# Performance work log

Hardware: AMD Instinct MI355X
Metric: run time of the kernel (lower is better)

Reference implementation:

```python
import jax, jax.numpy as jnp
import numpy as np

DT = 0.01          # oscillator integration step
GPI_TAU = 0.01     # gpi accumulation rate
NOISE_TAU = 1.0    # noise scale
MIN_OMEGA, MAX_OMEGA = 0.1, 1.0


def clinear(xr, xi, Wr, Wi, br, bi):
    # complex linear: (Wr + i Wi)(xr + i xi) + (br + i bi), weights stored [out, in]
    yr = xr @ Wr.T - xi @ Wi.T + br
    yi = xr @ Wi.T + xi @ Wr.T + bi
    return yr, yi


def crelu(yr, yi):
    # ReLU applied to real and imaginary parts independently
    return jax.nn.relu(yr), jax.nn.relu(yi)


def hopf_step(xr, xi, r, phi, omega):
    # Hopf oscillator in polar form, forced by complex input x = xr + i xi:
    #   dr   = dt * ( r(1 - r^2) + Re(x e^{-i phi}) )
    #   dphi = dt * ( omega + Im(x e^{-i phi}) / r )
    # output = r_new * e^{i phi_new}
    c, s = jnp.cos(phi), jnp.sin(phi)
    r_new = r + DT * (r * (1.0 - r * r) + xr * c + xi * s)
    phi_new = phi + DT * (omega + (xi * c - xr * s) / jnp.maximum(r, 1e-6))
    return r_new * jnp.cos(phi_new), r_new * jnp.sin(phi_new), r_new, phi_new


def setup_inputs() -> dict:
    T, D, U, A = 4096, 256, 2048, 64
    key = jax.random.key(0)
    ks = jax.random.split(key, 16)

    def lin(k, out_d, in_d):
        k1, k2, k3, k4 = jax.random.split(k, 4)
        sc = 1.0 / np.sqrt(in_d)
        return (jax.random.normal(k1, (out_d, in_d), dtype=jnp.float32) * sc,
                jax.random.normal(k2, (out_d, in_d), dtype=jnp.float32) * sc,
                jax.random.normal(k3, (out_d,), dtype=jnp.float32) * sc,
                jax.random.normal(k4, (out_d,), dtype=jnp.float32) * sc)

    l1Wr, l1Wi, l1br, l1bi = lin(ks[0], U, D)
    dpWr, dpWi, dpbr, dpbi = lin(ks[1], A, U)
    ipWr, ipWi, ipbr, ipbi = lin(ks[2], A, U)
    cWr, cWi, cbr, cbi = lin(ks[3], 1, U)
    return {
        'state': jax.random.normal(ks[4], (T, 1, D), dtype=jnp.float32),
        'phi1_init': jax.random.uniform(ks[5], (1, U), dtype=jnp.float32),
        'phi2_init': jax.random.uniform(ks[6], (1, U), dtype=jnp.float32),
        'noise_u': jax.random.uniform(ks[7], (T, A), dtype=jnp.float32),
        'omega1': jax.random.uniform(ks[8], (U,), minval=MIN_OMEGA, maxval=MAX_OMEGA, dtype=jnp.float32),
        'omega2': jax.random.uniform(ks[9], (U,), minval=MIN_OMEGA, maxval=MAX_OMEGA, dtype=jnp.float32),
        'l1Wr': l1Wr, 'l1Wi': l1Wi, 'l1br': l1br, 'l1bi': l1bi,
        'dpWr': dpWr, 'dpWi': dpWi, 'dpbr': dpbr, 'dpbi': dpbi,
        'ipWr': ipWr, 'ipWi': ipWi, 'ipbr': ipbr, 'ipbi': ipbi,
        'cWr': cWr, 'cWi': cWi, 'cbr': cbr, 'cbi': cbi,
    }


def reference(state, phi1_init, phi2_init, noise_u, omega1, omega2,
              l1Wr, l1Wi, l1br, l1bi, dpWr, dpWi, dpbr, dpbi,
              ipWr, ipWi, ipbr, ipbi, cWr, cWi, cbr, cbi):
    U = l1Wr.shape[0]
    A = dpWr.shape[0]
    carry0 = (jnp.ones((1, U)), phi1_init * 0.1,   # r1, phi1 (torch.rand/10)
              jnp.ones((1, U)), phi2_init * 0.1,   # r2, phi2
              jnp.zeros((1, A)),                   # gpi
              jnp.zeros((1, 1)))                   # p_value

    def step(carry, xs):
        r1, phi1, r2, phi2, gpi, p_value = carry
        s_t, nz_t = xs  # s_t: [1, D], nz_t: [A]
        # x = cReLU(l1(complex(state[t], state[t])))
        xr, xi = crelu(*clinear(s_t, s_t, l1Wr, l1Wi, l1br, l1bi))
        d1r, d1i, r1, phi1 = hopf_step(xr, xi, r1, phi1, omega1)
        d2r, d2i, r2, phi2 = hopf_step(xr, xi, r2, phi2, omega2)
        vr, vi = clinear(d1r, d1i, cWr, cWi, cbr, cbi)
        value = jnp.sqrt(vr * vr + vi * vi)          # |critic(d1out)|  [1,1]
        delta_V = value - p_value                    # pd_flag = sc_flag = 0
        lD1 = jax.nn.sigmoid(5.0 * delta_V)
        lD2 = jax.nn.sigmoid(-5.0 * delta_V)
        dpr, dpi = crelu(*clinear(d1r * lD1, d1i * lD1, dpWr, dpWi, dpbr, dpbi))
        ipr, ipi = crelu(*clinear(d2r * lD2, d2i * lD2, ipWr, ipWi, ipbr, ipbi))
        noise = NOISE_TAU * (nz_t[None, :] * 2.0 * lD2 - lD2)  # real-valued, adds to real part
        diff_r = dpr - (ipr + noise)
        diff_i = dpi - ipi
        gpi = gpi + GPI_TAU * jnp.sqrt(diff_r * diff_r + diff_i * diff_i)
        return (r1, phi1, r2, phi2, gpi, value), (gpi, value)

    (r1, phi1, r2, phi2, gpi, value), (gpi_traj, value_traj) = jax.lax.scan(
        step, carry0, (state, noise_u))
    probs = jax.nn.softmax(gpi, axis=1)
    return probs, value, gpi_traj
```

## Files before the change

### kernel.cpp

```cpp
#include <hip/hip_runtime.h>
#include <hip/hip_bf16.h>
#include <string.h>
#include <stdint.h>


#define T_ 4096
#define D_ 256
#define U_ 2048
#define A_ 64

typedef float f32x4 __attribute__((ext_vector_type(4)));
typedef short bh8 __attribute__((ext_vector_type(8)));
union F8 { uint32_t u[4]; bh8 v; };

__device__ __forceinline__ float bflo(uint32_t p) { return __uint_as_float(p << 16); }
__device__ __forceinline__ float bfhi(uint32_t p) { return __uint_as_float(p & 0xffff0000u); }
__device__ __forceinline__ uint16_t bf16rne(float x) {
  __hip_bfloat16 h = __float2bfloat16(x);
  uint16_t u;
  __builtin_memcpy(&u, &h, 2);
  return u;
}

#define HOPF_LOAD(BUF, i, tbase)                                            \
  do {                                                                      \
    const float* bx_ = xc + (size_t)((tbase) + (i)) * (U_ * 2);             \
    asm volatile("global_load_dwordx2 %0, %1, %2"                           \
                 : "=v"(BUF[i])                                             \
                 : "v"(voffx), "s"(bx_));                                   \
  } while (0)

#define HOPF_STEP(BUF, i, tb)                                               \
  do {                                                                      \
    const float xr_ = BUF[i].x, xi_ = BUF[i].y;                             \
    const float f_ = fmaf(xr_, c, xi_ * s);                                 \
    const float g_ = fmaf(xi_, c, -(xr_ * s));                              \
    const float rn_ = fmaf(0.01f, fmaf(r, fmaf(-r, r, 1.0f), f_), r);       \
    const float rinv_ = __builtin_amdgcn_rcpf(fmaxf(r, 1e-6f));             \
    const float phin_ = fmaf(0.01f, g_ * rinv_, phi + dto);                 \
    float cn_, sn_;                                                         \
    __sincosf(phin_, &sn_, &cn_);                                           \
    uint32_t pk_;                                                           \
    asm("v_cvt_pk_bf16_f32 %0, %1, %2"                                     \
        : "=v"(pk_)                                                         \
        : "v"(rn_ * cn_), "v"(rn_ * sn_));                                  \
    const uint32_t* bd_ = dst + (size_t)((tb) + (i)) * U_;                  \
    asm volatile("global_store_dword %0, %1, %2" ::"v"(voffd), "v"(pk_),    \
                 "s"(bd_));                                                  \
    r = rn_; phi = phin_; c = cn_; s = sn_;                                 \
  } while (0)

#define VMWAIT(N)                                  \
  asm volatile("s_waitcnt vmcnt(" #N ")");         \
  __builtin_amdgcn_sched_barrier(0)

#define WAIT_TILE(tt)                                                       \
  do {                                                                      \
    uint32_t rdy_;                                                          \
    for (;;) {                                                              \
      rdy_ = 0u;                                                            \
      if (threadIdx.x == 0)                                                 \
        rdy_ = __hip_atomic_fetch_add(&flags[tt], 0u, __ATOMIC_RELAXED,     \
                                      __HIP_MEMORY_SCOPE_AGENT);            \
      rdy_ = __shfl(rdy_, 0);                                               \
      if (rdy_ >= 32u) break;                                               \
      __builtin_amdgcn_s_sleep(8);                                          \
    }                                                                       \
    __builtin_amdgcn_sched_barrier(0);                                      \
  } while (0)

__global__ __launch_bounds__(256) void k_fused(
    const float* __restrict__ S, const float* __restrict__ Wr,
    const float* __restrict__ Wi, const float* __restrict__ br,
    const float* __restrict__ bi, const float* __restrict__ phi1,
    const float* __restrict__ phi2, const float* __restrict__ om1,
    const float* __restrict__ om2, float* __restrict__ xc,
    uint32_t* __restrict__ d1c, uint32_t* __restrict__ d2c,
    uint32_t* __restrict__ flags) {
  const int bid = blockIdx.x;
  if (bid >= 64) {
    __shared__ float sT[32][68];
    __shared__ float wrT[32][68];
    __shared__ float wiT[32][68];
    const int tid = threadIdx.x;
    const int gb = bid - 64;
    const int t0 = (gb >> 5) * 64;
    const int u0 = (gb & 31) * 64;
    const int un = tid & 15, tm = tid >> 4;
    const int lr = tid >> 3;
    const int lc = (tid & 7) * 4;
    float accR[4][4] = {}, accI[4][4] = {};
    for (int k0 = 0; k0 < D_; k0 += 32) {
      __syncthreads();
#pragma unroll
      for (int p = 0; p < 2; ++p) {
        const int row = p * 32 + lr;
        float4 v = *(const float4*)&S[(size_t)(t0 + row) * D_ + k0 + lc];
        sT[lc + 0][row] = v.x; sT[lc + 1][row] = v.y;
        sT[lc + 2][row] = v.z; sT[lc + 3][row] = v.w;
        float4 a = *(const float4*)&Wr[(size_t)(u0 + row) * D_ + k0 + lc];
        wrT[lc + 0][row] = a.x; wrT[lc + 1][row] = a.y;
        wrT[lc + 2][row] = a.z; wrT[lc + 3][row] = a.w;
        float4 b = *(const float4*)&Wi[(size_t)(u0 + row) * D_ + k0 + lc];
        wiT[lc + 0][row] = b.x; wiT[lc + 1][row] = b.y;
        wiT[lc + 2][row] = b.z; wiT[lc + 3][row] = b.w;
      }
      __syncthreads();
#pragma unroll
      for (int k = 0; k < 32; ++k) {
        const float4 sv = *(const float4*)&sT[k][tm * 4];
        const float4 ar = *(const float4*)&wrT[k][un * 4];
        const float4 ai = *(const float4*)&wiT[k][un * 4];
        const float ss[4] = {sv.x, sv.y, sv.z, sv.w};
        const float wd[4] = {ar.x - ai.x, ar.y - ai.y, ar.z - ai.z, ar.w - ai.w};
        const float wm[4] = {ar.x + ai.x, ar.y + ai.y, ar.z + ai.z, ar.w + ai.w};
#pragma unroll
        for (int i = 0; i < 4; ++i)
#pragma unroll
          for (int j = 0; j < 4; ++j) {
            accR[i][j] = fmaf(ss[i], wd[j], accR[i][j]);
            accI[i][j] = fmaf(ss[i], wm[j], accI[i][j]);
          }
      }
    }
    const float4 brv = *(const float4*)&br[u0 + un * 4];
    const float4 biv = *(const float4*)&bi[u0 + un * 4];
    const float brx[4] = {brv.x, brv.y, brv.z, brv.w};
    const float bix[4] = {biv.x, biv.y, biv.z, biv.w};
#pragma unroll
    for (int i = 0; i < 4; ++i) {
      float vr[4], vi[4];
#pragma unroll
      for (int j = 0; j < 4; ++j) {
        vr[j] = fmaxf(accR[i][j] + brx[j], 0.f);
        vi[j] = fmaxf(accI[i][j] + bix[j], 0.f);
      }
      const size_t base = ((size_t)(t0 + tm * 4 + i) * U_ + u0 + un * 4) * 2;
      f32x4 lo = {vr[0], vi[0], vr[1], vi[1]};
      f32x4 hi = {vr[2], vi[2], vr[3], vi[3]};
      float* p0 = &xc[base];
      float* p1 = &xc[base + 4];
      asm volatile("global_store_dwordx4 %0, %1, off sc1" ::"v"(p0), "v"(lo)
                   : "memory");
      asm volatile("global_store_dwordx4 %0, %1, off sc1" ::"v"(p1), "v"(hi)
                   : "memory");
    }
    asm volatile("s_waitcnt vmcnt(0)");
    __syncthreads();
    if (tid == 0)
      __hip_atomic_fetch_add(&flags[t0 >> 6], 1u, __ATOMIC_RELAXED,
                             __HIP_MEMORY_SCOPE_AGENT);
    return;
  }
  if (threadIdx.x >= 64) return;
  __builtin_amdgcn_s_setprio(3);
  const int ub = bid & 31;
  const int osc = bid >> 5;
  const int u = ub * 64 + threadIdx.x;
  float phi = (osc ? phi2[u] : phi1[u]) * 0.1f;
  const float omega = osc ? om2[u] : om1[u];
  const uint32_t* __restrict__ dst = (osc ? d2c : d1c);
  const float dto = 0.01f * omega;
  float r = 1.0f;
  float c, s;
  __sincosf(phi, &s, &c);
  const uint32_t voffx = (uint32_t)u * 8u;
  const uint32_t voffd = (uint32_t)u * 4u;

  constexpr int PF = 32;
  float2 bufA[PF], bufB[PF];
  WAIT_TILE(0);
#pragma unroll
  for (int i = 0; i < PF; ++i) HOPF_LOAD(bufA, i, 0);
#pragma unroll
  for (int i = 0; i < PF; ++i) HOPF_LOAD(bufB, i, PF);
  VMWAIT(32);

  for (int t0 = 0; t0 < T_; t0 += 2 * PF) {
#pragma unroll
    for (int i = 0; i < PF; ++i) HOPF_STEP(bufA, i, t0);
    {
      int tp = t0 + 2 * PF;
      if (tp >= T_) tp = 0;
      WAIT_TILE(tp >> 6);
#pragma unroll
      for (int i = 0; i < PF; ++i) HOPF_LOAD(bufA, i, tp);
    }
    VMWAIT(63);
#pragma unroll
    for (int i = 0; i < PF; ++i) HOPF_STEP(bufB, i, t0 + PF);
    {
      int tp = t0 + 3 * PF;
      if (tp >= T_) tp = 0;
#pragma unroll
      for (int i = 0; i < PF; ++i) HOPF_LOAD(bufB, i, tp);
    }
    VMWAIT(63);
  }
  asm volatile("s_waitcnt vmcnt(0)");
  __builtin_amdgcn_s_setprio(0);
}

__global__ __launch_bounds__(256) void k_crit_wcvt(
    const uint32_t* __restrict__ d1c, const float* __restrict__ cWr,
    const float* __restrict__ cWi, const float* __restrict__ cbr,
    const float* __restrict__ cbi, const float* __restrict__ dpWr,
    const float* __restrict__ dpWi, const float* __restrict__ ipWr,
    const float* __restrict__ ipWi, float* __restrict__ value,
    uint16_t* __restrict__ wc) {
  const int tid = threadIdx.x;
  if (blockIdx.x >= T_) {
    const float* srcs[4] = {dpWr, dpWi, ipWr, ipWi};
    const int g = (blockIdx.x - T_) * 256 + tid;
#pragma unroll
    for (int mi = 0; mi < 4; ++mi) {
      const float* sp = srcs[mi];
      uint16_t* hi = wc + (size_t)(2 * mi) * 131072;
      uint16_t* lo = wc + (size_t)(2 * mi + 1) * 131072;
      for (int j = 0; j < 32; ++j) {
        const int e = g * 32 + j;
        const float w = sp[e];
        const uint16_t hb = bf16rne(w);
        const float hf = __uint_as_float((uint32_t)hb << 16);
        hi[e] = hb;
        lo[e] = bf16rne(w - hf);
      }
    }
    return;
  }
  const int t = blockIdx.x;
  float vr = 0.f, vi = 0.f;
#pragma unroll
  for (int i = 0; i < 8; ++i) {
    const int uu = i * 256 + tid;
    const uint32_t p = d1c[(size_t)t * U_ + uu];
    const float dr = bflo(p), di = bfhi(p);
    const float wr = cWr[uu], wi = cWi[uu];
    vr = fmaf(dr, wr, fmaf(-di, wi, vr));
    vi = fmaf(dr, wi, fmaf(di, wr, vi));
  }
#pragma unroll
  for (int o = 32; o >= 1; o >>= 1) {
    vr += __shfl_xor(vr, o);
    vi += __shfl_xor(vi, o);
  }
  __shared__ float red[2][4];
  if ((tid & 63) == 0) { red[0][tid >> 6] = vr; red[1][tid >> 6] = vi; }
  __syncthreads();
  if (tid == 0) {
    const float r0 = red[0][0] + red[0][1] + red[0][2] + red[0][3] + cbr[0];
    const float i0 = red[1][0] + red[1][1] + red[1][2] + red[1][3] + cbi[0];
    value[t] = sqrtf(r0 * r0 + i0 * i0);
  }
}

#define MFMA_(A, B, C) \
  __builtin_amdgcn_mfma_f32_16x16x32_bf16((A).v, (B).v, (C), 0, 0, 0)

__global__ __launch_bounds__(256) void k_gemmDm_ld(
    const uint32_t* __restrict__ d1c, const uint32_t* __restrict__ d2c,
    const uint16_t* __restrict__ wc, const float* __restrict__ value,
    float* __restrict__ m, float* __restrict__ lD1,
    float* __restrict__ lD2) {
  const int tid = threadIdx.x;
  const int bid = blockIdx.x;
  if (bid >= 256) {
    const int t = (bid - 256) * 256 + tid;
    const float v = value[t];
    const float pv = (t > 0) ? value[t - 1] : 0.f;
    const float x = 5.0f * (v - pv);
    const float sg = 1.0f / (1.0f + __expf(-x));
    lD1[t] = sg;
    lD2[t] = 1.0f - sg;
    return;
  }
  const int w = tid >> 6;
  const int l = tid & 63;
  const int t0 = bid * 16;
  const int a0 = w * 16;
  const int lr15 = l & 15;
  const int g4 = (l >> 4) * 4;
  const uint32_t* d1p = d1c + (size_t)(t0 + lr15) * U_ + g4;
  const uint32_t* d2p = d2c + (size_t)(t0 + lr15) * U_ + g4;
  const size_t wbase = (size_t)(a0 + lr15) * U_ + g4;
  const uint16_t* w0 = wc + wbase;
  f32x4 acc0 = {0.f, 0.f, 0.f, 0.f};
  f32x4 acc1 = {0.f, 0.f, 0.f, 0.f};
  f32x4 acc2 = {0.f, 0.f, 0.f, 0.f};
  f32x4 acc3 = {0.f, 0.f, 0.f, 0.f};
  for (int kk = 0; kk < U_; kk += 32) {
    const uint4 da = *(const uint4*)(d1p + kk);
    const uint4 db = *(const uint4*)(d1p + kk + 16);
    F8 fr1, fi1, f1n;
    fr1.u[0] = (da.x & 0xffffu) | (da.y << 16);
    fr1.u[1] = (da.z & 0xffffu) | (da.w << 16);
    fr1.u[2] = (db.x & 0xffffu) | (db.y << 16);
    fr1.u[3] = (db.z & 0xffffu) | (db.w << 16);
    fi1.u[0] = (da.x >> 16) | (da.y & 0xffff0000u);
    fi1.u[1] = (da.z >> 16) | (da.w & 0xffff0000u);
    fi1.u[2] = (db.x >> 16) | (db.y & 0xffff0000u);
    fi1.u[3] = (db.z >> 16) | (db.w & 0xffff0000u);
    f1n.u[0] = fi1.u[0] ^ 0x80008000u; f1n.u[1] = fi1.u[1] ^ 0x80008000u;
    f1n.u[2] = fi1.u[2] ^ 0x80008000u; f1n.u[3] = fi1.u[3] ^ 0x80008000u;
    const uint4 dc = *(const uint4*)(d2p + kk);
    const uint4 dd = *(const uint4*)(d2p + kk + 16);
    F8 fr2, fi2, f2n;
    fr2.u[0] = (dc.x & 0xffffu) | (dc.y << 16);
    fr2.u[1] = (dc.z & 0xffffu) | (dc.w << 16);
    fr2.u[2] = (dd.x & 0xffffu) | (dd.y << 16);
    fr2.u[3] = (dd.z & 0xffffu) | (dd.w << 16);
    fi2.u[0] = (dc.x >> 16) | (dc.y & 0xffff0000u);
    fi2.u[1] = (dc.z >> 16) | (dc.w & 0xffff0000u);
    fi2.u[2] = (dd.x >> 16) | (dd.y & 0xffff0000u);
    fi2.u[3] = (dd.z >> 16) | (dd.w & 0xffff0000u);
    f2n.u[0] = fi2.u[0] ^ 0x80008000u; f2n.u[1] = fi2.u[1] ^ 0x80008000u;
    f2n.u[2] = fi2.u[2] ^ 0x80008000u; f2n.u[3] = fi2.u[3] ^ 0x80008000u;
    F8 wf[8];
#pragma unroll
    for (int ai = 0; ai < 8; ++ai) {
      const uint16_t* bp = w0 + (size_t)ai * 131072 + kk;
      const uint2 x0 = *(const uint2*)bp;
      const uint2 x1 = *(const uint2*)(bp + 16);
      wf[ai].u[0] = x0.x; wf[ai].u[1] = x0.y;
      wf[ai].u[2] = x1.x; wf[ai].u[3] = x1.y;
    }
    acc0 = MFMA_(fr1, wf[0], acc0); acc0 = MFMA_(fr1, wf[1], acc0);
    acc0 = MFMA_(f1n, wf[2], acc0); acc0 = MFMA_(f1n, wf[3], acc0);
    acc1 = MFMA_(fr1, wf[2], acc1); acc1 = MFMA_(fr1, wf[3], acc1);
    acc1 = MFMA_(fi1, wf[0], acc1); acc1 = MFMA_(fi1, wf[1], acc1);
    acc2 = MFMA_(fr2, wf[4], acc2); acc2 = MFMA_(fr2, wf[5], acc2);
    acc2 = MFMA_(f2n, wf[6], acc2); acc2 = MFMA_(f2n, wf[7], acc2);
    acc3 = MFMA_(fr2, wf[6], acc3); acc3 = MFMA_(fr2, wf[7], acc3);
    acc3 = MFMA_(fi2, wf[4], acc3); acc3 = MFMA_(fi2, wf[5], acc3);
  }
  const size_t MS = (size_t)T_ * A_;
#pragma unroll
  for (int reg = 0; reg < 4; ++reg) {
    const int t = t0 + (l >> 4) * 4 + reg;
    const size_t o = (size_t)t * A_ + a0 + lr15;
    m[0 * MS + o] = acc0[reg];
    m[1 * MS + o] = acc1[reg];
    m[2 * MS + o] = acc2[reg];
    m[3 * MS + o] = acc3[reg];
  }
}

__global__ __launch_bounds__(256) void k_epi(
    const float* __restrict__ m4, const float* __restrict__ lD1,
    const float* __restrict__ lD2, const float* __restrict__ noise,
    const float* __restrict__ dpbr, const float* __restrict__ dpbi,
    const float* __restrict__ ipbr, const float* __restrict__ ipbi,
    float* __restrict__ nrm) {
  const size_t MS = (size_t)T_ * A_;
  const int gid = blockIdx.x * 256 + threadIdx.x;
  const size_t e0 = (size_t)gid * 4;
  const int t = (int)(e0 >> 6);
  const int a0 = (int)(e0 & 63);
  float m[4][4];
#pragma unroll
  for (int mi = 0; mi < 4; ++mi) {
    const float4 v = *(const float4*)&m4[(size_t)mi * MS + e0];
    m[mi][0] = v.x; m[mi][1] = v.y; m[mi][2] = v.z; m[mi][3] = v.w;
  }
  const float l1 = lD1[t], l2 = lD2[t];
  const float4 nzv = *(const float4*)&noise[e0];
  const float nz[4] = {nzv.x, nzv.y, nzv.z, nzv.w};
  const float4 q1 = *(const float4*)&dpbr[a0];
  const float4 q2 = *(const float4*)&dpbi[a0];
  const float4 q3 = *(const float4*)&ipbr[a0];
  const float4 q4 = *(const float4*)&ipbi[a0];
  const float b1r[4] = {q1.x, q1.y, q1.z, q1.w};
  const float b1i[4] = {q2.x, q2.y, q2.z, q2.w};
  const float b2r[4] = {q3.x, q3.y, q3.z, q3.w};
  const float b2i[4] = {q4.x, q4.y, q4.z, q4.w};
  float res[4];
#pragma unroll
  for (int j = 0; j < 4; ++j) {
    const float dpr = fmaxf(fmaf(l1, m[0][j], b1r[j]), 0.f);
    const float dpi = fmaxf(fmaf(l1, m[1][j], b1i[j]), 0.f);
    const float ipr = fmaxf(fmaf(l2, m[2][j], b2r[j]), 0.f);
    const float ipi = fmaxf(fmaf(l2, m[3][j], b2i[j]), 0.f);
    const float nzs = l2 * (2.f * nz[j] - 1.f);
    const float dr = dpr - ipr - nzs;
    const float di = dpi - ipi;
    res[j] = sqrtf(dr * dr + di * di);
  }
  *(float4*)&nrm[e0] = make_float4(res[0], res[1], res[2], res[3]);
}

__global__ __launch_bounds__(64) void k_scan_part(const float* __restrict__ nrm,
                                                  float* __restrict__ csum) {
  const int c = blockIdx.x;
  const int a = threadIdx.x;
  const int tb = c * 64;
  float run = 0.f;
  for (int i = 0; i < 64; ++i) run += nrm[(size_t)(tb + i) * 64 + a];
  csum[c * 64 + a] = run;
}

__global__ __launch_bounds__(64) void k_scan_mid(const float* __restrict__ csum,
                                                 const float* __restrict__ value,
                                                 float* __restrict__ coff,
                                                 float* __restrict__ out) {
  const int a = threadIdx.x;
  float acc = 0.f;
#pragma unroll
  for (int cc = 0; cc < 64; ++cc) {
    coff[cc * 64 + a] = acc;
    acc += csum[cc * 64 + a];
  }
  const float g = 0.01f * acc;
  float mx = g;
#pragma unroll
  for (int o = 32; o >= 1; o >>= 1) mx = fmaxf(mx, __shfl_xor(mx, o));
  const float e = __expf(g - mx);
  float sm = e;
#pragma unroll
  for (int o = 32; o >= 1; o >>= 1) sm += __shfl_xor(sm, o);
  out[a] = e / sm;
  if (a == 0) out[64] = value[T_ - 1];
}

__global__ __launch_bounds__(64) void k_scan_out(const float* __restrict__ nrm,
                                                 const float* __restrict__ coff,
                                                 float* __restrict__ out) {
  const int c = blockIdx.x;
  const int a = threadIdx.x;
  const int tb = c * 64;
  float off = coff[c * 64 + a];
  float* o65 = out + 65;
  for (int i = 0; i < 64; ++i) {
    off += nrm[(size_t)(tb + i) * 64 + a];
    o65[(size_t)(tb + i) * 64 + a] = 0.01f * off;
  }
}

extern "C" void kernel_launch(void* const* d_in, const int* in_sizes, int n_in,
                              void* d_out, int out_size, void* d_ws,
                              size_t ws_size, hipStream_t stream) {
  const float* state = (const float*)d_in[0];
  const float* phi1 = (const float*)d_in[1];
  const float* phi2 = (const float*)d_in[2];
  const float* noise = (const float*)d_in[3];
  const float* om1 = (const float*)d_in[4];
  const float* om2 = (const float*)d_in[5];
  const float* l1Wr = (const float*)d_in[6];
  const float* l1Wi = (const float*)d_in[7];
  const float* l1br = (const float*)d_in[8];
  const float* l1bi = (const float*)d_in[9];
  const float* dpWr = (const float*)d_in[10];
  const float* dpWi = (const float*)d_in[11];
  const float* dpbr = (const float*)d_in[12];
  const float* dpbi = (const float*)d_in[13];
  const float* ipWr = (const float*)d_in[14];
  const float* ipWi = (const float*)d_in[15];
  const float* ipbr = (const float*)d_in[16];
  const float* ipbi = (const float*)d_in[17];
  const float* cWr = (const float*)d_in[18];
  const float* cWi = (const float*)d_in[19];
  const float* cbr = (const float*)d_in[20];
  const float* cbi = (const float*)d_in[21];
  float* out = (float*)d_out;

  char* ws = (char*)d_ws;
  float* xc = (float*)(ws + (size_t)0);
  uint32_t* d1c = (uint32_t*)(ws + (size_t)67108864);
  uint32_t* d2c = (uint32_t*)(ws + (size_t)100663296);
  float* m4 = (float*)(ws + (size_t)0);
  uint16_t* wc = (uint16_t*)(ws + (size_t)4194304);
  float* nrm = (float*)(ws + (size_t)16777216);
  float* value = (float*)(ws + (size_t)17825792);
  float* lD1 = (float*)(ws + (size_t)17825792 + 16384);
  float* lD2 = (float*)(ws + (size_t)17825792 + 32768);
  float* csum = (float*)(ws + (size_t)17825792 + 49152);
  float* coff = (float*)(ws + (size_t)17825792 + 65536);
  uint32_t* flags = (uint32_t*)out;

  hipMemsetAsync(out, 0, 256, stream);
  k_fused<<<64 + (T_ / 64) * (U_ / 64), 256, 0, stream>>>(
      state, l1Wr, l1Wi, l1br, l1bi, phi1, phi2, om1, om2, xc, d1c, d2c,
      flags);
  k_crit_wcvt<<<T_ + 16, 256, 0, stream>>>(d1c, cWr, cWi, cbr, cbi, dpWr,
                                           dpWi, ipWr, ipWi, value, wc);
  k_gemmDm_ld<<<256 + 16, 256, 0, stream>>>(d1c, d2c, wc, value, m4, lD1,
                                            lD2);
  k_epi<<<256, 256, 0, stream>>>(m4, lD1, lD2, noise, dpbr, dpbi, ipbr, ipbi,
                                 nrm);
  k_scan_part<<<64, 64, 0, stream>>>(nrm, csum);
  k_scan_mid<<<1, 64, 0, stream>>>(csum, value, coff, out);
  k_scan_out<<<64, 64, 0, stream>>>(nrm, coff, out);
}
```

Measured before the change: 543.3 us.

## Pre-swizzle split-bf16 weights into fragment order and stage activations via LDS

```diff
diff --git a/kernel.cpp b/kernel.cpp
--- a/kernel.cpp
+++ b/kernel.cpp
@@ -211,20 +211,43 @@
   const int tid = threadIdx.x;
   if (blockIdx.x >= T_) {
     const float* srcs[4] = {dpWr, dpWi, ipWr, ipWi};
-    const int g = (blockIdx.x - T_) * 256 + tid;
-#pragma unroll
-    for (int mi = 0; mi < 4; ++mi) {
-      const float* sp = srcs[mi];
-      uint16_t* hi = wc + (size_t)(2 * mi) * 131072;
-      uint16_t* lo = wc + (size_t)(2 * mi + 1) * 131072;
-      for (int j = 0; j < 32; ++j) {
-        const int e = g * 32 + j;
-        const float w = sp[e];
-        const uint16_t hb = bf16rne(w);
-        const float hf = __uint_as_float((uint32_t)hb << 16);
-        hi[e] = hb;
-        lo[e] = bf16rne(w - hf);
-      }
+    const int wgid = (blockIdx.x - T_) * 4 + (tid >> 6);
+    const int l = tid & 63;
+    const int lr15 = l & 15;
+    const int g4 = (l >> 4) * 4;
+    for (int i = 0; i < 16; ++i) {
+      const int task = wgid * 16 + i;
+      const int mi = task >> 8;
+      const int st = (task >> 6) & 3;
+      const int ch = task & 63;
+      const float* sp = srcs[mi] + (size_t)(st * 16 + lr15) * U_ + ch * 32 + g4;
+      float w0 = sp[0], w1 = sp[1], w2 = sp[2], w3 = sp[3];
+      float w4 = sp[16], w5 = sp[17], w6 = sp[18], w7 = sp[19];
+      const uint16_t h0 = bf16rne(w0), h1 = bf16rne(w1), h2 = bf16rne(w2),
+                     h3 = bf16rne(w3), h4 = bf16rne(w4), h5 = bf16rne(w5),
+                     h6 = bf16rne(w6), h7 = bf16rne(w7);
+      uint4 hv;
+      hv.x = (uint32_t)h0 | ((uint32_t)h1 << 16);
+      hv.y = (uint32_t)h2 | ((uint32_t)h3 << 16);
+      hv.z = (uint32_t)h4 | ((uint32_t)h5 << 16);
+      hv.w = (uint32_t)h6 | ((uint32_t)h7 << 16);
+      const uint16_t q0 = bf16rne(w0 - __uint_as_float((uint32_t)h0 << 16));
+      const uint16_t q1 = bf16rne(w1 - __uint_as_float((uint32_t)h1 << 16));
+      const uint16_t q2 = bf16rne(w2 - __uint_as_float((uint32_t)h2 << 16));
+      const uint16_t q3 = bf16rne(w3 - __uint_as_float((uint32_t)h3 << 16));
+      const uint16_t q4 = bf16rne(w4 - __uint_as_float((uint32_t)h4 << 16));
+      const uint16_t q5 = bf16rne(w5 - __uint_as_float((uint32_t)h5 << 16));
+      const uint16_t q6 = bf16rne(w6 - __uint_as_float((uint32_t)h6 << 16));
+      const uint16_t q7 = bf16rne(w7 - __uint_as_float((uint32_t)h7 << 16));
+      uint4 lv;
+      lv.x = (uint32_t)q0 | ((uint32_t)q1 << 16);
+      lv.y = (uint32_t)q2 | ((uint32_t)q3 << 16);
+      lv.z = (uint32_t)q4 | ((uint32_t)q5 << 16);
+      lv.w = (uint32_t)q6 | ((uint32_t)q7 << 16);
+      const size_t fhi = ((size_t)((2 * mi) * 4 + st) * 64 + ch);
+      const size_t flo = ((size_t)((2 * mi + 1) * 4 + st) * 64 + ch);
+      *(uint4*)(wc + (fhi << 9) + (l << 3)) = hv;
+      *(uint4*)(wc + (flo << 9) + (l << 3)) = lv;
     }
     return;
   }
@@ -274,23 +297,33 @@
     lD2[t] = 1.0f - sg;
     return;
   }
+  __shared__ __align__(16) uint32_t d1T[16][36];
+  __shared__ __align__(16) uint32_t d2T[16][36];
   const int w = tid >> 6;
   const int l = tid & 63;
   const int t0 = bid * 16;
   const int a0 = w * 16;
   const int lr15 = l & 15;
   const int g4 = (l >> 4) * 4;
-  const uint32_t* d1p = d1c + (size_t)(t0 + lr15) * U_ + g4;
-  const uint32_t* d2p = d2c + (size_t)(t0 + lr15) * U_ + g4;
-  const size_t wbase = (size_t)(a0 + lr15) * U_ + g4;
-  const uint16_t* w0 = wc + wbase;
+  const int sid = tid & 127;
+  const int srow = sid >> 3;
+  const int scol = (sid & 7) * 4;
+  const uint32_t* sbase = (tid < 128 ? d1c : d2c) + (size_t)(t0 + srow) * U_ + scol;
   f32x4 acc0 = {0.f, 0.f, 0.f, 0.f};
   f32x4 acc1 = {0.f, 0.f, 0.f, 0.f};
   f32x4 acc2 = {0.f, 0.f, 0.f, 0.f};
   f32x4 acc3 = {0.f, 0.f, 0.f, 0.f};
   for (int kk = 0; kk < U_; kk += 32) {
-    const uint4 da = *(const uint4*)(d1p + kk);
-    const uint4 db = *(const uint4*)(d1p + kk + 16);
+    __syncthreads();
+    {
+      const uint4 v = *(const uint4*)(sbase + kk);
+      uint32_t(*dT)[36] = (tid < 128) ? d1T : d2T;
+      dT[srow][scol + 0] = v.x; dT[srow][scol + 1] = v.y;
+      dT[srow][scol + 2] = v.z; dT[srow][scol + 3] = v.w;
+    }
+    __syncthreads();
+    const uint4 da = *(const uint4*)&d1T[lr15][g4];
+    const uint4 db = *(const uint4*)&d1T[lr15][16 + g4];
     F8 fr1, fi1, f1n;
     fr1.u[0] = (da.x & 0xffffu) | (da.y << 16);
     fr1.u[1] = (da.z & 0xffffu) | (da.w << 16);
@@ -302,8 +335,8 @@
     fi1.u[3] = (db.z >> 16) | (db.w & 0xffff0000u);
     f1n.u[0] = fi1.u[0] ^ 0x80008000u; f1n.u[1] = fi1.u[1] ^ 0x80008000u;
     f1n.u[2] = fi1.u[2] ^ 0x80008000u; f1n.u[3] = fi1.u[3] ^ 0x80008000u;
-    const uint4 dc = *(const uint4*)(d2p + kk);
-    const uint4 dd = *(const uint4*)(d2p + kk + 16);
+    const uint4 dc = *(const uint4*)&d2T[lr15][g4];
+    const uint4 dd = *(const uint4*)&d2T[lr15][16 + g4];
     F8 fr2, fi2, f2n;
     fr2.u[0] = (dc.x & 0xffffu) | (dc.y << 16);
     fr2.u[1] = (dc.z & 0xffffu) | (dc.w << 16);
@@ -316,13 +349,14 @@
     f2n.u[0] = fi2.u[0] ^ 0x80008000u; f2n.u[1] = fi2.u[1] ^ 0x80008000u;
     f2n.u[2] = fi2.u[2] ^ 0x80008000u; f2n.u[3] = fi2.u[3] ^ 0x80008000u;
     F8 wf[8];
+    const int ch = kk >> 5;
 #pragma unroll
     for (int ai = 0; ai < 8; ++ai) {
-      const uint16_t* bp = w0 + (size_t)ai * 131072 + kk;
-      const uint2 x0 = *(const uint2*)bp;
-      const uint2 x1 = *(const uint2*)(bp + 16);
-      wf[ai].u[0] = x0.x; wf[ai].u[1] = x0.y;
-      wf[ai].u[2] = x1.x; wf[ai].u[3] = x1.y;
+      const uint4 x =
+          *(const uint4*)(wc + (((size_t)(ai * 4 + w) * 64 + ch) << 9) +
+                          (l << 3));
+      wf[ai].u[0] = x.x; wf[ai].u[1] = x.y;
+      wf[ai].u[2] = x.z; wf[ai].u[3] = x.w;
     }
     acc0 = MFMA_(fr1, wf[0], acc0); acc0 = MFMA_(fr1, wf[1], acc0);
     acc0 = MFMA_(f1n, wf[2], acc0); acc0 = MFMA_(f1n, wf[3], acc0);
```

After: 465.0 us. -14.4%, faster.
